# Optimization experiments

Measured on AMD Instinct MI355X. Metric: run time of the kernel, lower is better.

Reference implementation:

```python
import jax, jax.numpy as jnp
import numpy as np

GN_EPS = 1e-6
NUM_GROUPS = 32


def group_norm(x, gamma, beta):
    # x: [B,H,W,C], normalize per-sample over (H,W, C//G) within each of G groups
    B, H, W, C = x.shape
    G = NUM_GROUPS
    xg = x.reshape(B, H, W, G, C // G)
    mean = jnp.mean(xg, axis=(1, 2, 4), keepdims=True)
    var = jnp.var(xg, axis=(1, 2, 4), keepdims=True)
    xg = (xg - mean) * jax.lax.rsqrt(var + GN_EPS)
    x = xg.reshape(B, H, W, C)
    return x * gamma + beta


def setup_inputs() -> dict:
    key = jax.random.key(0)
    ks = jax.random.split(key, 6)
    B, H, W, C = 4, 64, 64, 512
    scale = 1.0 / np.sqrt(C)
    return {
        "x": jax.random.normal(ks[0], (B, H, W, C), jnp.float32),
        "gn_gamma": jnp.ones((C,), jnp.float32),
        "gn_beta": jnp.zeros((C,), jnp.float32),
        "Wq": jax.random.normal(ks[1], (C, C), jnp.float32) * scale,
        "bq": jnp.zeros((C,), jnp.float32),
        "Wk": jax.random.normal(ks[2], (C, C), jnp.float32) * scale,
        "bk": jnp.zeros((C,), jnp.float32),
        "Wv": jax.random.normal(ks[3], (C, C), jnp.float32) * scale,
        "bv": jnp.zeros((C,), jnp.float32),
        "Wo": jax.random.normal(ks[4], (C, C), jnp.float32) * scale,
        "bo": jnp.zeros((C,), jnp.float32),
    }


def reference(x, gn_gamma, gn_beta, Wq, bq, Wk, bk, Wv, bv, Wo, bo):
    B, H, W, C = x.shape
    h = group_norm(x, gn_gamma, gn_beta)          # [B,H,W,C]
    t = h.reshape(B, H * W, C)                     # flatten spatial tokens
    q = t @ Wq + bq                                # [B,N,C]
    k = t @ Wk + bk
    v = t @ Wv + bv
    scores = jnp.einsum('bnc,bmc->bnm', q, k) * (C ** -0.5)  # [B,N,N]
    attn = jax.nn.softmax(scores, axis=-1)
    out = jnp.einsum('bnm,bmc->bnc', attn, v)      # [B,N,C]
    out = out @ Wo + bo
    return out.reshape(B, H, W, C) + x
```

## Files before the change

### kernel.cpp

```cpp
#include <hip/hip_runtime.h>
#include <stdint.h>

using u16 = unsigned short;
typedef __attribute__((ext_vector_type(8))) short short8;
typedef __attribute__((ext_vector_type(4))) float floatx4;

__device__ __forceinline__ float b2f(u16 s) {
    union { unsigned u; float f; } x; x.u = ((unsigned)s) << 16; return x.f;
}
__device__ __forceinline__ u16 f2b(float f) {
    unsigned u = __float_as_uint(f);
    unsigned r = (u + 0x7fffu + ((u >> 16) & 1u)) >> 16;
    return (u16)r;
}

__device__ __forceinline__ void gl16(const u16* g, u16* l) {
    __builtin_amdgcn_global_load_lds((const __attribute__((address_space(1))) void*)g,
                                     (__attribute__((address_space(3))) void*)l,
                                     16, 0, 0);
}

__global__ __launch_bounds__(256) void gn_stats_k(const float* __restrict__ x,
                                                  float* __restrict__ stats) {
    int bg = blockIdx.x;
    int b = bg >> 5, g = bg & 31;
    const size_t base = (size_t)b * 4096 * 512 + g * 16;
    int t = threadIdx.x;
    float s = 0.f, ss = 0.f;
    for (int it = 0; it < 64; ++it) {
        int vi = it * 256 + t;
        int n = vi >> 2;
        int j = (vi & 3) * 4;
        float4 u = *(const float4*)(x + base + (size_t)n * 512 + j);
        s += u.x + u.y + u.z + u.w;
        ss += u.x * u.x + u.y * u.y + u.z * u.z + u.w * u.w;
    }
    for (int off = 32; off; off >>= 1) {
        s  += __shfl_down(s, off, 64);
        ss += __shfl_down(ss, off, 64);
    }
    __shared__ float rs[4], rss[4];
    int lane = t & 63, w = t >> 6;
    if (lane == 0) { rs[w] = s; rss[w] = ss; }
    __syncthreads();
    if (t == 0) {
        float S1 = rs[0] + rs[1] + rs[2] + rs[3];
        float S2 = rss[0] + rss[1] + rss[2] + rss[3];
        float mean = S1 * (1.f / 65536.f);
        float var  = S2 * (1.f / 65536.f) - mean * mean;
        stats[2 * bg]     = mean;
        stats[2 * bg + 1] = rsqrtf(var + 1e-6f);
    }
}

__global__ __launch_bounds__(256) void gn_apply_k(const float* __restrict__ x,
                                                  const float* __restrict__ gamma,
                                                  const float* __restrict__ beta,
                                                  const float* __restrict__ stats,
                                                  u16* __restrict__ h) {
    size_t v = (size_t)blockIdx.x * 256 + threadIdx.x;
    size_t e = v * 4;
    int c = (int)(e & 511);
    int b = (int)(e >> 21);
    int g = c >> 4;
    float mean = stats[2 * (b * 32 + g)];
    float rstd = stats[2 * (b * 32 + g) + 1];
    float4 xv = *(const float4*)(x + e);
    float4 gv = *(const float4*)(gamma + c);
    float4 bv = *(const float4*)(beta + c);
    ushort4 o;
    o.x = f2b((xv.x - mean) * rstd * gv.x + bv.x);
    o.y = f2b((xv.y - mean) * rstd * gv.y + bv.y);
    o.z = f2b((xv.z - mean) * rstd * gv.z + bv.z);
    o.w = f2b((xv.w - mean) * rstd * gv.w + bv.w);
    *(ushort4*)(h + e) = o;
}

__global__ __launch_bounds__(256) void transpose_f2b(const float* __restrict__ src,
                                                     u16* __restrict__ dst) {
    __shared__ float tile[32][33];
    int tx = threadIdx.x, ty = threadIdx.y;
    int r0 = blockIdx.x * 32, c0 = blockIdx.y * 32;
#pragma unroll
    for (int i = 0; i < 4; ++i)
        tile[ty + i * 8][tx] = src[(size_t)(r0 + ty + i * 8) * 512 + c0 + tx];
    __syncthreads();
#pragma unroll
    for (int i = 0; i < 4; ++i)
        dst[(size_t)(c0 + ty + i * 8) * 512 + r0 + tx] = f2b(tile[tx][ty + i * 8]);
}

__global__ __launch_bounds__(256) void transpose_b2b(const u16* __restrict__ src,
                                                     u16* __restrict__ dst,
                                                     int src_ld, int dst_ld,
                                                     long long sSrc, long long sDst) {
    __shared__ u16 tile[32][33];
    src += (size_t)blockIdx.z * sSrc;
    dst += (size_t)blockIdx.z * sDst;
    int tx = threadIdx.x, ty = threadIdx.y;
    int r0 = blockIdx.x * 32, c0 = blockIdx.y * 32;
#pragma unroll
    for (int i = 0; i < 4; ++i)
        tile[ty + i * 8][tx] = src[(size_t)(r0 + ty + i * 8) * src_ld + c0 + tx];
    __syncthreads();
#pragma unroll
    for (int i = 0; i < 4; ++i)
        dst[(size_t)(c0 + ty + i * 8) * dst_ld + r0 + tx] = tile[tx][ty + i * 8];
}

__global__ __launch_bounds__(256) void concat_bias_f(const float* __restrict__ bq,
                                                     const float* __restrict__ bk,
                                                     const float* __restrict__ bv,
                                                     float* __restrict__ dst) {
    int i = blockIdx.x * 256 + threadIdx.x;
    const float* src = (i < 512) ? bq : (i < 1024) ? bk : bv;
    dst[i] = src[i & 511];
}

__global__ __launch_bounds__(256) void gemm_bt(const u16* __restrict__ A, int lda,
                                               const u16* __restrict__ B, int ldb,
                                               u16* __restrict__ C, float* __restrict__ Cf,
                                               int ldc,
                                               const float* __restrict__ bias,
                                               const float* __restrict__ resid,
                                               int K, float scale) {
    __shared__ u16 As[128 * 32];
    __shared__ u16 Bs[128 * 32];
    const int t = threadIdx.x;
    const int lane = t & 63, w = t >> 6;
    const int wm = (w >> 1) * 64, wn = (w & 1) * 64;
    const int r = lane & 15, q = lane >> 4;
    const int m0 = blockIdx.x * 128;
    const int n0 = blockIdx.y * 128;

    floatx4 acc[4][4];
#pragma unroll
    for (int mi = 0; mi < 4; ++mi)
#pragma unroll
        for (int ni = 0; ni < 4; ++ni) acc[mi][ni] = (floatx4){0.f, 0.f, 0.f, 0.f};

    const int srow = lane >> 2;
    const int scol = (lane & 3) * 8;
    const u16* gA = A + (size_t)(m0 + w * 32 + srow) * lda + scol;
    const u16* gB = B + (size_t)(n0 + w * 32 + srow) * ldb + scol;
    u16* lA = As + w * 1024;
    u16* lB = Bs + w * 1024;

    for (int k0 = 0; k0 < K; k0 += 32) {
        __syncthreads();
        gl16(gA,                     lA);
        gl16(gA + (size_t)16 * lda,  lA + 512);
        gl16(gB,                     lB);
        gl16(gB + (size_t)16 * ldb,  lB + 512);
        gA += 32; gB += 32;
        __syncthreads();
        short8 af[4], bfr[4];
#pragma unroll
        for (int mi = 0; mi < 4; ++mi)
            af[mi] = *(const short8*)(As + (wm + mi * 16 + r) * 32 + q * 8);
#pragma unroll
        for (int ni = 0; ni < 4; ++ni)
            bfr[ni] = *(const short8*)(Bs + (wn + ni * 16 + r) * 32 + q * 8);
#pragma unroll
        for (int mi = 0; mi < 4; ++mi)
#pragma unroll
            for (int ni = 0; ni < 4; ++ni)
                acc[mi][ni] = __builtin_amdgcn_mfma_f32_16x16x32_bf16(af[mi], bfr[ni],
                                                                      acc[mi][ni], 0, 0, 0);
    }

#pragma unroll
    for (int ni = 0; ni < 4; ++ni) {
        int col = n0 + wn + ni * 16 + r;
        float bv = bias ? bias[col] : 0.f;
#pragma unroll
        for (int mi = 0; mi < 4; ++mi) {
            int rowb = m0 + wm + mi * 16 + q * 4;
#pragma unroll
            for (int i = 0; i < 4; ++i) {
                size_t off = (size_t)(rowb + i) * ldc + col;
                float v = acc[mi][ni][i] * scale + bv;
                if (resid) v += resid[off];
                if (Cf) Cf[off] = v;
                else    C[off] = f2b(v);
            }
        }
    }
}

#define FLASH_SMEM 147968
__global__ __launch_bounds__(512, 2) void flash_k(const u16* __restrict__ qkv,
                                                  const u16* __restrict__ vt,
                                                  u16* __restrict__ ao) {
    extern __shared__ u16 smem[];
    u16* Ks = smem;
    u16* Vs = smem + 32768;
    u16* Pl = smem + 65536;
    float* lex = (float*)(smem + 73728);
    const int t = threadIdx.x;
    const int lane = t & 63, w = t >> 6;
    const int rw = w & 3, kh = w >> 2;
    const int r = lane & 15, q = lane >> 4;
    const int swz = (q ^ ((r >> 1) & 3)) * 8;
    const int b = blockIdx.y, qt = blockIdx.x;
    const u16* qb = qkv + (size_t)b * 4096 * 1536;
    const u16* kb = qb + 512;
    const u16* vb = vt + (size_t)b * 512 * 4096;
    u16* aob = ao + (size_t)b * 4096 * 512;
    const int wch = w * 64;

    auto stageK = [&](int buf, int kt, int g) {
#pragma unroll
        for (int j = 0; j < 4; ++j) {
            int u = t + j * 512;
            int key = (u & 511) >> 2;
            int sub = u >> 9;
            int c = ((u & 3) ^ ((key >> 1) & 3)) * 8;
            gl16(kb + (size_t)(kt * 128 + key) * 1536 + g * 128 + sub * 32 + c,
                 Ks + buf * 16384 + u * 8);
        }
    };
    auto stageV = [&](int buf, int kt, int k) {
#pragma unroll
        for (int j = 0; j < 4; ++j) {
            int u = t + j * 512;
            int ch = u >> 2;
            int c = ((u & 3) ^ ((ch >> 1) & 3)) * 8;
            gl16(vb + (size_t)ch * 4096 + kt * 128 + k * 32 + c,
                 Vs + buf * 16384 + u * 8);
        }
    };

    stageK(0, 0, 0);
    stageV(0, 0, 0);

    const int qrow = qt * 64 + rw * 16 + r;
    short8 Qreg[16];
#pragma unroll
    for (int kit = 0; kit < 16; ++kit)
        Qreg[kit] = *(const short8*)(qb + (size_t)qrow * 1536 + kit * 32 + q * 8);

    floatx4 acc_o[16];
#pragma unroll
    for (int i = 0; i < 16; ++i) acc_o[i] = (floatx4){0.f, 0.f, 0.f, 0.f};
    float l_half = 0.f;
    const float sc2 = 0.06375872f;

    for (int kt = 0; kt < 32; ++kt) {
        floatx4 acc_s[4];
#pragma unroll
        for (int mi = 0; mi < 4; ++mi) acc_s[mi] = (floatx4){0.f, 0.f, 0.f, 0.f};
#pragma unroll
        for (int g = 0; g < 4; ++g) {
            __syncthreads();
            if (g < 3) stageK((g + 1) & 1, kt, g + 1);
            const u16* kbase = Ks + (g & 1) * 16384;
#pragma unroll
            for (int s = 0; s < 4; ++s) {
                const u16* sbase = kbase + s * 4096;
#pragma unroll
                for (int mi = 0; mi < 4; ++mi) {
                    short8 af = *(const short8*)(sbase + (kh * 64 + mi * 16 + r) * 32 + swz);
                    acc_s[mi] = __builtin_amdgcn_mfma_f32_16x16x32_bf16(
                        af, Qreg[g * 4 + s], acc_s[mi], 0, 0, 0);
                }
            }
        }
        float rs = 0.f;
#pragma unroll
        for (int mi = 0; mi < 4; ++mi)
#pragma unroll
            for (int i = 0; i < 4; ++i) {
                float pv = __builtin_amdgcn_exp2f(acc_s[mi][i] * sc2);
                acc_s[mi][i] = pv;
                rs += pv;
            }
        rs += __shfl_xor(rs, 16, 64);
        rs += __shfl_xor(rs, 32, 64);
        l_half += rs;
#pragma unroll
        for (int mi = 0; mi < 4; ++mi) {
            uint2 vv;
            vv.x = (unsigned)f2b(acc_s[mi][0]) | ((unsigned)f2b(acc_s[mi][1]) << 16);
            vv.y = (unsigned)f2b(acc_s[mi][2]) | ((unsigned)f2b(acc_s[mi][3]) << 16);
            *(uint2*)(Pl + (rw * 16 + r) * 128 +
                      (((kh * 8 + 2 * mi + (q >> 1)) ^ (r & 7)) * 8) + (q & 1) * 4) = vv;
        }
#pragma unroll
        for (int k = 0; k < 4; ++k) {
            __syncthreads();
            if (k < 3)        stageV((k + 1) & 1, kt, k + 1);
            else if (kt < 31) stageV(0, kt + 1, 0);
            if (k == 0 && kt < 31) stageK(0, kt + 1, 0);
            short8 ap[4];
#pragma unroll
            for (int mi = 0; mi < 4; ++mi)
                ap[mi] = *(const short8*)(Pl + (mi * 16 + r) * 128 +
                                          (((k * 4 + q) ^ (r & 7)) * 8));
            const u16* vbase = Vs + (k & 1) * 16384;
#pragma unroll
            for (int ni = 0; ni < 4; ++ni) {
                short8 bf = *(const short8*)(vbase + (wch + ni * 16 + r) * 32 + swz);
#pragma unroll
                for (int mi = 0; mi < 4; ++mi)
                    acc_o[mi * 4 + ni] = __builtin_amdgcn_mfma_f32_16x16x32_bf16(
                        ap[mi], bf, acc_o[mi * 4 + ni], 0, 0, 0);
            }
        }
    }
    if (q == 0) lex[w * 16 + r] = l_half;
    __syncthreads();
#pragma unroll
    for (int mi = 0; mi < 4; ++mi) {
        float4 la = *(const float4*)(lex + mi * 16 + q * 4);
        float4 lb = *(const float4*)(lex + 64 + mi * 16 + q * 4);
        float i0 = 1.f / (la.x + lb.x), i1 = 1.f / (la.y + lb.y);
        float i2 = 1.f / (la.z + lb.z), i3 = 1.f / (la.w + lb.w);
        int rowb = qt * 64 + mi * 16 + q * 4;
#pragma unroll
        for (int ni = 0; ni < 4; ++ni) {
            int col = wch + ni * 16 + r;
            aob[(size_t)(rowb + 0) * 512 + col] = f2b(acc_o[mi * 4 + ni][0] * i0);
            aob[(size_t)(rowb + 1) * 512 + col] = f2b(acc_o[mi * 4 + ni][1] * i1);
            aob[(size_t)(rowb + 2) * 512 + col] = f2b(acc_o[mi * 4 + ni][2] * i2);
            aob[(size_t)(rowb + 3) * 512 + col] = f2b(acc_o[mi * 4 + ni][3] * i3);
        }
    }
}

extern "C" void kernel_launch(void* const* d_in, const int* in_sizes, int n_in,
                              void* d_out, int out_size, void* d_ws, size_t ws_size,
                              hipStream_t stream) {
    const float* x     = (const float*)d_in[0];
    const float* gamma = (const float*)d_in[1];
    const float* beta  = (const float*)d_in[2];
    const float* Wq    = (const float*)d_in[3];
    const float* bq    = (const float*)d_in[4];
    const float* Wk    = (const float*)d_in[5];
    const float* bk    = (const float*)d_in[6];
    const float* Wv    = (const float*)d_in[7];
    const float* bv    = (const float*)d_in[8];
    const float* Wo    = (const float*)d_in[9];
    const float* bo    = (const float*)d_in[10];
    float* out = (float*)d_out;

    char* ws = (char*)d_ws;
    float* stats  = (float*)(ws);
    float* bqkv   = (float*)(ws + 4096);
    u16*   wqkv_t = (u16*)(ws + 16384);
    u16*   wo_t   = wqkv_t + (size_t)1536 * 512;
    u16*   h      = wo_t + (size_t)512 * 512;
    u16*   qkv    = h   + (size_t)16384 * 512;
    u16*   vt     = qkv + (size_t)16384 * 1536;
    u16*   ao     = h;

    const long long sQKV = (long long)4096 * 1536;
    const long long sVT  = (long long)512 * 4096;

    dim3 tblk(32, 8, 1);
    transpose_f2b<<<dim3(16, 16, 1), tblk, 0, stream>>>(Wq, wqkv_t);
    transpose_f2b<<<dim3(16, 16, 1), tblk, 0, stream>>>(Wk, wqkv_t + 512 * 512);
    transpose_f2b<<<dim3(16, 16, 1), tblk, 0, stream>>>(Wv, wqkv_t + 1024 * 512);
    transpose_f2b<<<dim3(16, 16, 1), tblk, 0, stream>>>(Wo, wo_t);
    concat_bias_f<<<6, 256, 0, stream>>>(bq, bk, bv, bqkv);

    gn_stats_k<<<128, 256, 0, stream>>>(x, stats);
    gn_apply_k<<<8192, 256, 0, stream>>>(x, gamma, beta, stats, h);

    gemm_bt<<<dim3(128, 12, 1), 256, 0, stream>>>(h, 512, wqkv_t, 512,
                                                  qkv, nullptr, 1536, bqkv, nullptr,
                                                  512, 1.0f);
    transpose_b2b<<<dim3(128, 16, 4), tblk, 0, stream>>>(qkv + 1024, vt, 1536, 4096,
                                                         sQKV, sVT);
    hipFuncSetAttribute((const void*)flash_k,
                        hipFuncAttributeMaxDynamicSharedMemorySize, FLASH_SMEM);
    flash_k<<<dim3(64, 4, 1), 512, FLASH_SMEM, stream>>>(qkv, vt, ao);

    gemm_bt<<<dim3(128, 4, 1), 256, 0, stream>>>(ao, 512, wo_t, 512,
                                                 nullptr, out, 512, bo, x,
                                                 512, 1.0f);
}
```

Measured before the change: 425.1 us.

## Fuse V transpose into QKV GEMM epilogue and batch weight transposes

The QKV GEMM epilogue now writes V tiles directly in transposed [B,C,N] layout, which removes the separate bf16 transpose kernel and its round trip through global memory. The four weight transpose launches are merged into a single launch indexed by blockIdx.z. The transposed V stores are 8-byte writes strided by the sequence length, so they coalesce less well than row-major stores.

```diff
diff --git a/kernel.cpp b/kernel.cpp
--- a/kernel.cpp
+++ b/kernel.cpp
@@ -76,8 +76,15 @@
     *(ushort4*)(h + e) = o;
 }
 
-__global__ __launch_bounds__(256) void transpose_f2b(const float* __restrict__ src,
-                                                     u16* __restrict__ dst) {
+__global__ __launch_bounds__(256) void transpose_f2b4(const float* __restrict__ Wq,
+                                                      const float* __restrict__ Wk,
+                                                      const float* __restrict__ Wv,
+                                                      const float* __restrict__ Wo,
+                                                      u16* __restrict__ wqkv_t,
+                                                      u16* __restrict__ wo_t) {
+    int z = blockIdx.z;
+    const float* src = (z == 0) ? Wq : (z == 1) ? Wk : (z == 2) ? Wv : Wo;
+    u16* dst = (z < 3) ? wqkv_t + (size_t)z * 512 * 512 : wo_t;
     __shared__ float tile[32][33];
     int tx = threadIdx.x, ty = threadIdx.y;
     int r0 = blockIdx.x * 32, c0 = blockIdx.y * 32;
@@ -88,24 +95,6 @@
 #pragma unroll
     for (int i = 0; i < 4; ++i)
         dst[(size_t)(c0 + ty + i * 8) * 512 + r0 + tx] = f2b(tile[tx][ty + i * 8]);
-}
-
-__global__ __launch_bounds__(256) void transpose_b2b(const u16* __restrict__ src,
-                                                     u16* __restrict__ dst,
-                                                     int src_ld, int dst_ld,
-                                                     long long sSrc, long long sDst) {
-    __shared__ u16 tile[32][33];
-    src += (size_t)blockIdx.z * sSrc;
-    dst += (size_t)blockIdx.z * sDst;
-    int tx = threadIdx.x, ty = threadIdx.y;
-    int r0 = blockIdx.x * 32, c0 = blockIdx.y * 32;
-#pragma unroll
-    for (int i = 0; i < 4; ++i)
-        tile[ty + i * 8][tx] = src[(size_t)(r0 + ty + i * 8) * src_ld + c0 + tx];
-    __syncthreads();
-#pragma unroll
-    for (int i = 0; i < 4; ++i)
-        dst[(size_t)(c0 + ty + i * 8) * dst_ld + r0 + tx] = tile[tx][ty + i * 8];
 }
 
 __global__ __launch_bounds__(256) void concat_bias_f(const float* __restrict__ bq,
@@ -123,6 +112,7 @@
                                                int ldc,
                                                const float* __restrict__ bias,
                                                const float* __restrict__ resid,
+                                               u16* __restrict__ Vt,
                                                int K, float scale) {
     __shared__ u16 As[128 * 32];
     __shared__ u16 Bs[128 * 32];
@@ -169,6 +159,7 @@
                                                                       acc[mi][ni], 0, 0, 0);
     }
 
+    const bool vpath = (Vt != nullptr) && (n0 >= 1024);
 #pragma unroll
     for (int ni = 0; ni < 4; ++ni) {
         int col = n0 + wn + ni * 16 + r;
@@ -176,13 +167,24 @@
 #pragma unroll
         for (int mi = 0; mi < 4; ++mi) {
             int rowb = m0 + wm + mi * 16 + q * 4;
-#pragma unroll
-            for (int i = 0; i < 4; ++i) {
-                size_t off = (size_t)(rowb + i) * ldc + col;
-                float v = acc[mi][ni][i] * scale + bv;
-                if (resid) v += resid[off];
-                if (Cf) Cf[off] = v;
-                else    C[off] = f2b(v);
+            if (vpath) {
+                int c = col - 1024;
+                int b = rowb >> 12, n = rowb & 4095;
+                ushort4 o;
+                o.x = f2b(acc[mi][ni][0] * scale + bv);
+                o.y = f2b(acc[mi][ni][1] * scale + bv);
+                o.z = f2b(acc[mi][ni][2] * scale + bv);
+                o.w = f2b(acc[mi][ni][3] * scale + bv);
+                *(ushort4*)(Vt + (((size_t)b * 512 + c) << 12) + n) = o;
+            } else {
+#pragma unroll
+                for (int i = 0; i < 4; ++i) {
+                    size_t off = (size_t)(rowb + i) * ldc + col;
+                    float v = acc[mi][ni][i] * scale + bv;
+                    if (resid) v += resid[off];
+                    if (Cf) Cf[off] = v;
+                    else    C[off] = f2b(v);
+                }
             }
         }
     }
@@ -354,14 +356,8 @@
     u16*   vt     = qkv + (size_t)16384 * 1536;
     u16*   ao     = h;
 
-    const long long sQKV = (long long)4096 * 1536;
-    const long long sVT  = (long long)512 * 4096;
-
     dim3 tblk(32, 8, 1);
-    transpose_f2b<<<dim3(16, 16, 1), tblk, 0, stream>>>(Wq, wqkv_t);
-    transpose_f2b<<<dim3(16, 16, 1), tblk, 0, stream>>>(Wk, wqkv_t + 512 * 512);
-    transpose_f2b<<<dim3(16, 16, 1), tblk, 0, stream>>>(Wv, wqkv_t + 1024 * 512);
-    transpose_f2b<<<dim3(16, 16, 1), tblk, 0, stream>>>(Wo, wo_t);
+    transpose_f2b4<<<dim3(16, 16, 4), tblk, 0, stream>>>(Wq, Wk, Wv, Wo, wqkv_t, wo_t);
     concat_bias_f<<<6, 256, 0, stream>>>(bq, bk, bv, bqkv);
 
     gn_stats_k<<<128, 256, 0, stream>>>(x, stats);
@@ -369,14 +365,12 @@
 
     gemm_bt<<<dim3(128, 12, 1), 256, 0, stream>>>(h, 512, wqkv_t, 512,
                                                   qkv, nullptr, 1536, bqkv, nullptr,
-                                                  512, 1.0f);
-    transpose_b2b<<<dim3(128, 16, 4), tblk, 0, stream>>>(qkv + 1024, vt, 1536, 4096,
-                                                         sQKV, sVT);
+                                                  vt, 512, 1.0f);
     hipFuncSetAttribute((const void*)flash_k,
                         hipFuncAttributeMaxDynamicSharedMemorySize, FLASH_SMEM);
     flash_k<<<dim3(64, 4, 1), 512, FLASH_SMEM, stream>>>(qkv, vt, ao);
 
     gemm_bt<<<dim3(128, 4, 1), 256, 0, stream>>>(ao, 512, wo_t, 512,
                                                  nullptr, out, 512, bo, x,
-                                                 512, 1.0f);
-}
+                                                 nullptr, 512, 1.0f);
+}
```

Result: faster. 406.2 us (-4.5%).
